# Performance work log

Hardware: AMD Instinct MI355X
Metric: run time of the kernel (lower is better)

The kernel has to match this reference:

```python
import jax, jax.numpy as jnp
import numpy as np

BS, CK, H, W, T = 4, 64, 32, 32, 16
HW = H * W
N = T * HW
CV = 256
TOP_K = 30


def setup_inputs() -> dict:
    key = jax.random.key(0)
    ks = jax.random.split(key, 16)
    inp = {
        'query_key': jax.random.normal(ks[0], (BS, CK, H, W), jnp.float32),
        'query_selection': jax.random.uniform(ks[1], (BS, CK, H, W), jnp.float32),
        'pix_feat': jax.random.normal(ks[2], (BS, CV, H, W), jnp.float32),
        'sensory': jax.random.normal(ks[3], (BS, CV, H, W), jnp.float32),
        'last_mask': jax.random.uniform(ks[4], (BS, 1, H, W), jnp.float32),
        'last_pix_feat': jax.random.normal(ks[5], (BS, CV, H, W), jnp.float32),
        'last_msk_value': jax.random.normal(ks[6], (BS, 1, CV, H, W), jnp.float32),
        'mem_key': jax.random.normal(ks[7], (BS, CK, N), jnp.float32),
        'mem_shrinkage': jax.random.uniform(ks[8], (BS, 1, N), jnp.float32),
        'mem_msk_value': jax.random.normal(ks[9], (BS, CV, N), jnp.float32),
        'mem_valid': jnp.ones((BS, N), jnp.float32),
        'obj_memory': jax.random.normal(ks[10], (BS, 1, 16, CV), jnp.float32),
        # uncertainty head proxy: 1x1 conv over concat(last_pix_feat, pix_feat, last_mask, diff)
        'W_uncert': jax.random.normal(ks[11], (1, CV + CV + 1 + CV), jnp.float32) * 0.02,
        'b_uncert': jnp.zeros((1,), jnp.float32),
    }
    return inp


def reference(query_key, query_selection, pix_feat, sensory, last_mask,
              last_pix_feat, last_msk_value, mem_key, mem_shrinkage,
              mem_msk_value, mem_valid, obj_memory, W_uncert, b_uncert):
    bs = query_key.shape[0]
    h, w = query_key.shape[-2:]
    hw = h * w
    qk = query_key.reshape(bs, CK, hw)            # [b,64,hw]
    qe = query_selection.reshape(bs, CK, hw)      # [b,64,hw]
    mk_t = jnp.swapaxes(mem_key, 1, 2)            # [b,N,64]
    # negative squared L2 distance, selection-weighted
    a_sq = jnp.einsum('bnc,bch->bnh', mk_t * mk_t, qe)
    two_ab = 2.0 * jnp.einsum('bnc,bch->bnh', mk_t, qk * qe)
    b_sq = jnp.sum(qe * qk * qk, axis=1, keepdims=True)     # [b,1,hw]
    sim = (-a_sq + two_ab - b_sq)                           # [b,N,hw]
    sim = sim * jnp.swapaxes(mem_shrinkage, 1, 2) / jnp.sqrt(jnp.float32(CK))
    sim = sim + (1.0 - mem_valid[..., None]) * -60000.0
    # top-k softmax over memory axis, scatter back to dense affinity
    sim_t = jnp.swapaxes(sim, 1, 2)                         # [b,hw,N]
    top_vals, top_idx = jax.lax.top_k(sim_t, TOP_K)         # [b,hw,k]
    probs = jax.nn.softmax(top_vals, axis=-1)
    b_ix = jnp.arange(bs)[:, None, None]
    q_ix = jnp.arange(hw)[None, :, None]
    aff = jnp.zeros_like(sim_t).at[b_ix, q_ix, top_idx].set(probs)  # [b,hw,N]
    visual = jnp.einsum('bcn,bhn->bch', mem_msk_value, aff).reshape(bs, 1, CV, h, w)
    # uncertainty-gated blend with last memory value (pred_uncertainty proxy: 1x1 conv)
    diff = visual[:, 0] - last_msk_value[:, 0]              # [b,256,h,w]
    feats = jnp.concatenate([last_pix_feat, pix_feat, last_mask, diff], axis=1)
    logits = jnp.einsum('bchw,oc->bohw', feats, W_uncert) + b_uncert[None, :, None, None]
    up = jax.nn.sigmoid(logits)[:, None]                    # [b,1,1,h,w]
    out = visual * up + last_msk_value * (1.0 - up)         # [b,1,256,h,w]
    return out
```

## Files before the change

kernel.cpp:

```cpp
#include <hip/hip_runtime.h>
#include <math.h>

#define BSZ 4
#define CKC 64
#define HWP 1024
#define NMEM 16384
#define CVC 256
#define PT 32
#define NT 128
#define NSPLIT 4
#define CHUNK (NMEM / NSPLIT)
#define NC (NSPLIT * 32)
#define PT2 16

#define WS_BQ_OFF    0
#define WS_BQ_SZ     (BSZ * 128 * HWP)
#define WS_BSQ_OFF   (WS_BQ_OFF + WS_BQ_SZ)
#define WS_BSQ_SZ    (BSZ * HWP)
#define WS_PRE_OFF   (WS_BSQ_OFF + WS_BSQ_SZ)
#define WS_PRE_SZ    (BSZ * HWP)
#define WS_PARTV_OFF (WS_PRE_OFF + WS_PRE_SZ)
#define WS_PARTV_SZ  (BSZ * HWP * NC)
#define WS_PARTI_OFF (WS_PARTV_OFF + WS_PARTV_SZ)
#define WS_PARTI_SZ  (BSZ * HWP * NC)
#define WS_VT_OFF    (WS_PARTI_OFF + WS_PARTI_SZ)
#define WS_VT_SZ     (BSZ * NMEM * CVC)
#define WS_TOTAL_FLOATS (WS_VT_OFF + WS_VT_SZ)

__global__ __launch_bounds__(256) void prep_kernel(
    const float* __restrict__ qk, const float* __restrict__ qe,
    const float* __restrict__ pf, const float* __restrict__ lm,
    const float* __restrict__ lpf, const float* __restrict__ lmv,
    const float* __restrict__ W, const float* __restrict__ bu,
    float* __restrict__ Bq, float* __restrict__ bsq, float* __restrict__ prelog)
{
    __shared__ float red[16][17];
    const int t  = threadIdx.x;
    const int b  = blockIdx.x >> 6;
    const int p0 = (blockIdx.x & 63) << 4;
    const int pp = t & 15;
    const int cg = t >> 4;
    const int p  = p0 + pp;

    const float* qkb = qk + (size_t)b * CKC * HWP;
    const float* qeb = qe + (size_t)b * CKC * HWP;
    float* Bqb = Bq + (size_t)b * 128 * HWP;

    float bs = 0.f;
    #pragma unroll
    for (int i = 0; i < 4; ++i) {
        const int cidx = (cg << 2) + i;
        const float k_ = qkb[cidx * HWP + p];
        const float e_ = qeb[cidx * HWP + p];
        Bqb[cidx * HWP + p]        = 2.f * k_ * e_;
        Bqb[(64 + cidx) * HWP + p] = -e_;
        bs += e_ * k_ * k_;
    }
    red[cg][pp] = bs;
    __syncthreads();
    if (t < 16) {
        float s = 0.f;
        #pragma unroll
        for (int g2 = 0; g2 < 16; ++g2) s += red[g2][t];
        bsq[b * HWP + p0 + t] = s;
    }
    const float* lpfb = lpf + (size_t)b * CVC * HWP;
    const float* pfb  = pf  + (size_t)b * CVC * HWP;
    const float* lmvb = lmv + (size_t)b * CVC * HWP;
    float lg = 0.f;
    #pragma unroll
    for (int i = 0; i < 16; ++i) {
        const int cidx = (cg << 4) + i;
        lg += W[cidx]       * lpfb[cidx * HWP + p];
        lg += W[256 + cidx] * pfb[cidx * HWP + p];
        lg -= W[513 + cidx] * lmvb[cidx * HWP + p];
    }
    __syncthreads();
    red[cg][pp] = lg;
    __syncthreads();
    if (t < 16) {
        float s = bu[0] + W[512] * lm[b * HWP + p0 + t];
        #pragma unroll
        for (int g2 = 0; g2 < 16; ++g2) s += red[g2][t];
        prelog[b * HWP + p0 + t] = s;
    }
}

__global__ __launch_bounds__(256) void transpose_v(const float* __restrict__ V,
                                                   float* __restrict__ VT)
{
    __shared__ float tile[32][33];
    const int b  = blockIdx.z;
    const int n0 = blockIdx.x << 5;
    const int c0 = blockIdx.y << 5;
    const int tx = threadIdx.x, ty = threadIdx.y;
    const float* Vb  = V  + (size_t)b * CVC * NMEM;
    float*       VTb = VT + (size_t)b * NMEM * CVC;
    #pragma unroll
    for (int i = 0; i < 32; i += 8)
        tile[ty + i][tx] = Vb[(size_t)(c0 + ty + i) * NMEM + n0 + tx];
    __syncthreads();
    #pragma unroll
    for (int i = 0; i < 32; i += 8)
        VTb[(size_t)(n0 + ty + i) * CVC + c0 + tx] = tile[tx][ty + i];
}

__global__ __launch_bounds__(256) void sim_topk_kernel(
    const float* __restrict__ mk, const float* __restrict__ shr,
    const float* __restrict__ valid, const float* __restrict__ Bq,
    const float* __restrict__ bsq,
    float* __restrict__ partV, float* __restrict__ partI)
{
    __shared__ float mkS[64][NT];
    __shared__ float fS[64][PT];
    __shared__ float gS[64][PT];
    __shared__ float heapV[PT][34];
    __shared__ int   heapI[PT][34];
    __shared__ float qV[PT][33];
    __shared__ int   qI[PT][33];
    __shared__ float shrS[NT];
    __shared__ float penS[NT];
    __shared__ float bsqS[PT];
    __shared__ int   qCnt[PT];
    __shared__ int   pendAny;

    const int t     = threadIdx.x;
    const int b     = blockIdx.x >> 7;
    const int pg    = (blockIdx.x >> 2) & 31;
    const int ns    = blockIdx.x & 3;
    const int p0    = pg << 5;
    const int nbase = ns * CHUNK;
    const int tn    = t & 31;
    const int tp    = t >> 5;

    const float* Bqb = Bq + (size_t)b * 128 * HWP;
    for (int idx = t; idx < 64 * PT; idx += 256) {
        const int c = idx >> 5, pp = idx & 31;
        fS[c][pp] = Bqb[c * HWP + p0 + pp];
        gS[c][pp] = Bqb[(64 + c) * HWP + p0 + pp];
    }
    if (t < PT) {
        bsqS[t] = bsq[b * HWP + p0 + t];
        qCnt[t] = 0;
    }
    if (t == 0) pendAny = 0;

    const float* mkb  = mk    + (size_t)b * CKC * NMEM;
    const float* shrb = shr   + (size_t)b * NMEM;
    const float* vlb  = valid + (size_t)b * NMEM;

    for (int ntile = 0; ntile < CHUNK / NT; ++ntile) {
        const int nstart = nbase + ntile * NT;
        if (t < NT) {
            shrS[t] = shrb[nstart + t] * 0.125f;
            penS[t] = (1.f - vlb[nstart + t]) * -60000.f;
        }
        #pragma unroll
        for (int k = 0; k < 8; ++k) {
            const int idx = t + (k << 8);
            const int row = idx >> 5;
            const int c4  = (idx & 31) << 2;
            *(float4*)&mkS[row][c4] =
                *(const float4*)&mkb[(size_t)row * NMEM + nstart + c4];
        }
        __syncthreads();

        float acc[4][4];
        #pragma unroll
        for (int i = 0; i < 4; ++i)
            #pragma unroll
            for (int j = 0; j < 4; ++j) acc[i][j] = 0.f;

        #pragma unroll 8
        for (int cc = 0; cc < 64; ++cc) {
            const float4 a4 = *(const float4*)&mkS[cc][tn << 2];
            const float4 f4 = *(const float4*)&fS[cc][tp << 2];
            const float4 g4 = *(const float4*)&gS[cc][tp << 2];
            const float m[4]  = {a4.x, a4.y, a4.z, a4.w};
            const float ff[4] = {f4.x, f4.y, f4.z, f4.w};
            const float gg[4] = {g4.x, g4.y, g4.z, g4.w};
            #pragma unroll
            for (int i = 0; i < 4; ++i) {
                const float mv = m[i];
                #pragma unroll
                for (int j = 0; j < 4; ++j) {
                    const float t1 = fmaf(mv, gg[j], ff[j]);
                    acc[i][j] = fmaf(mv, t1, acc[i][j]);
                }
            }
        }

        float simv[4][4];
        #pragma unroll
        for (int i = 0; i < 4; ++i) {
            const float sh = shrS[(tn << 2) + i];
            const float pe = penS[(tn << 2) + i];
            #pragma unroll
            for (int j = 0; j < 4; ++j)
                simv[i][j] = fmaf(acc[i][j] - bsqS[(tp << 2) + j], sh, pe);
        }

        unsigned pending = 0xFFFFu;
        if (ntile == 0) {
            if (tn < 8) {
                #pragma unroll
                for (int j = 0; j < 4; ++j) {
                    const int p = (tp << 2) + j;
                    #pragma unroll
                    for (int i = 0; i < 4; ++i) {
                        heapV[p][1 + (tn << 2) + i] = simv[i][j];
                        heapI[p][1 + (tn << 2) + i] = nbase + (tn << 2) + i;
                    }
                }
                pending = 0;
            }
            __syncthreads();
            if (t < PT) {
                for (int rt = 16; rt >= 1; --rt) {
                    const float v = heapV[t][rt];
                    const int  ix = heapI[t][rt];
                    int i = rt;
                    while (true) {
                        const int l = i << 1;
                        if (l > 32) break;
                        int m = l;
                        float vm = heapV[t][l];
                        if (l + 1 <= 32) {
                            const float vr = heapV[t][l + 1];
                            if (vr < vm) { m = l + 1; vm = vr; }
                        }
                        if (vm >= v) break;
                        heapV[t][i] = vm; heapI[t][i] = heapI[t][m];
                        i = m;
                    }
                    heapV[t][i] = v; heapI[t][i] = ix;
                }
            }
            __syncthreads();
        }

        while (true) {
            if (t == 0) pendAny = 0;
            if (t < PT) qCnt[t] = 0;
            __syncthreads();
            if (pending) {
                #pragma unroll
                for (int j = 0; j < 4; ++j) {
                    const int p = (tp << 2) + j;
                    const float mv = heapV[p][1];
                    #pragma unroll
                    for (int i = 0; i < 4; ++i) {
                        const unsigned bitm = 1u << ((j << 2) + i);
                        if (pending & bitm) {
                            const float v = simv[i][j];
                            if (v > mv) {
                                const int slot = atomicAdd(&qCnt[p], 1);
                                if (slot < 32) {
                                    qV[p][slot] = v;
                                    qI[p][slot] = nstart + (tn << 2) + i;
                                    pending &= ~bitm;
                                }
                            } else pending &= ~bitm;
                        }
                    }
                }
                if (pending) pendAny = 1;
            }
            __syncthreads();
            if (t < PT) {
                int cnt = qCnt[t]; if (cnt > 32) cnt = 32;
                for (int s = 0; s < cnt; ++s) {
                    const float v = qV[t][s];
                    if (v > heapV[t][1]) {
                        const int ix = qI[t][s];
                        int i = 1;
                        while (true) {
                            const int l = i << 1;
                            if (l > 32) break;
                            int m = l;
                            float vm = heapV[t][l];
                            if (l + 1 <= 32) {
                                const float vr = heapV[t][l + 1];
                                if (vr < vm) { m = l + 1; vm = vr; }
                            }
                            if (vm >= v) break;
                            heapV[t][i] = vm; heapI[t][i] = heapI[t][m];
                            i = m;
                        }
                        heapV[t][i] = v; heapI[t][i] = ix;
                    }
                }
            }
            __syncthreads();
            const int again = pendAny;
            __syncthreads();
            if (!again) break;
        }
    }

    for (int idx = t; idx < PT * 32; idx += 256) {
        const int p = idx >> 5, s = idx & 31;
        const size_t gp = (size_t)b * HWP + p0 + p;
        partV[gp * NC + ns * 32 + s] = heapV[p][1 + s];
        partI[gp * NC + ns * 32 + s] = (float)heapI[p][1 + s];
    }
}

__global__ __launch_bounds__(256) void merge_kernel(
    const float* __restrict__ partV, const float* __restrict__ partI,
    const float* __restrict__ Vv, const float* __restrict__ lmv,
    const float* __restrict__ prelog, const float* __restrict__ W,
    float* __restrict__ out, int use_vt)
{
    __shared__ float candV[PT2][NC + 1];
    __shared__ int   candI[PT2][NC + 1];
    __shared__ float hV[PT2][34];
    __shared__ int   hI[PT2][34];
    __shared__ float probS[PT2][33];
    __shared__ int   selS[PT2][33];
    __shared__ float prelS[PT2];
    __shared__ float partS[4][PT2];
    __shared__ float upS[PT2];
    __shared__ float visS[CVC][PT2 + 1];

    const int t  = threadIdx.x;
    const int b  = blockIdx.x >> 6;
    const int pg = blockIdx.x & 63;
    const int p0 = pg << 4;

    for (int idx = t; idx < PT2 * NC; idx += 256) {
        const int p = idx >> 7, s = idx & (NC - 1);
        const size_t gp = (size_t)b * HWP + p0 + p;
        candV[p][s] = partV[gp * NC + s];
        candI[p][s] = (int)partI[gp * NC + s];
    }
    if (t < PT2) prelS[t] = prelog[b * HWP + p0 + t];
    __syncthreads();

    if (t < PT2) {
        const int p = t;
        #pragma unroll
        for (int s = 0; s < 32; ++s) { hV[p][1 + s] = candV[p][s]; hI[p][1 + s] = candI[p][s]; }
        for (int rt = 16; rt >= 1; --rt) {
            const float v = hV[p][rt]; const int ix = hI[p][rt];
            int i = rt;
            while (true) {
                const int l = i << 1;
                if (l > 32) break;
                int m = l;
                float vm = hV[p][l];
                if (l + 1 <= 32) { const float vr = hV[p][l + 1]; if (vr < vm) { m = l + 1; vm = vr; } }
                if (vm >= v) break;
                hV[p][i] = vm; hI[p][i] = hI[p][m];
                i = m;
            }
            hV[p][i] = v; hI[p][i] = ix;
        }
        for (int s = 32; s < NC; ++s) {
            const float v = candV[p][s];
            if (v > hV[p][1]) {
                const int ix = candI[p][s];
                int i = 1;
                while (true) {
                    const int l = i << 1;
                    if (l > 32) break;
                    int m = l;
                    float vm = hV[p][l];
                    if (l + 1 <= 32) { const float vr = hV[p][l + 1]; if (vr < vm) { m = l + 1; vm = vr; } }
                    if (vm >= v) break;
                    hV[p][i] = vm; hI[p][i] = hI[p][m];
                    i = m;
                }
                hV[p][i] = v; hI[p][i] = ix;
            }
        }
        const int m1 = 1;
        const int m2 = (hV[p][3] < hV[p][2]) ? 3 : 2;
        float mx = hV[p][1];
        #pragma unroll
        for (int s = 2; s <= 32; ++s) mx = fmaxf(mx, hV[p][s]);
        float sum = 0.f;
        #pragma unroll
        for (int s = 1; s <= 32; ++s) {
            const float e = (s == m1 || s == m2) ? 0.f : expf(hV[p][s] - mx);
            probS[p][s - 1] = e; sum += e;
            selS[p][s - 1]  = hI[p][s];
        }
        const float inv = 1.f / sum;
        #pragma unroll
        for (int s = 0; s < 32; ++s) probS[p][s] *= inv;
    }
    __syncthreads();

    const int c  = t;
    const int ln = t & 63;
    const int wv = t >> 6;
    float vis[PT2];
    const float* Vb = Vv + (use_vt ? (size_t)b * NMEM * CVC : (size_t)b * CVC * NMEM);
    #pragma unroll
    for (int p = 0; p < PT2; ++p) {
        float a = 0.f;
        for (int s = 0; s < 32; ++s) {
            const float pr = probS[p][s];
            if (pr != 0.f) {
                const int idx = selS[p][s];
                const float v = use_vt ? Vb[(size_t)idx * CVC + c]
                                       : Vb[(size_t)c * NMEM + idx];
                a = fmaf(pr, v, a);
            }
        }
        vis[p] = a;
        visS[c][p] = a;
    }
    const float w3 = W[513 + c];
    #pragma unroll
    for (int p = 0; p < PT2; ++p) {
        float v = w3 * vis[p];
        #pragma unroll
        for (int off = 32; off > 0; off >>= 1) v += __shfl_xor(v, off, 64);
        if (ln == 0) partS[wv][p] = v;
    }
    __syncthreads();
    if (t < PT2) {
        const float lg = prelS[t] + partS[0][t] + partS[1][t] + partS[2][t] + partS[3][t];
        upS[t] = 1.f / (1.f + expf(-lg));
    }
    __syncthreads();

    const int pp = t & 15;
    const int cg = t >> 4;
    const float u = upS[pp];
    #pragma unroll
    for (int ci = 0; ci < 16; ++ci) {
        const int cc = (cg << 4) + ci;
        const float vv = visS[cc][pp];
        const size_t off = ((size_t)b * CVC + cc) * HWP + p0 + pp;
        out[off] = vv * u + lmv[off] * (1.f - u);
    }
}

extern "C" void kernel_launch(void* const* d_in, const int* in_sizes, int n_in,
                              void* d_out, int out_size, void* d_ws, size_t ws_size,
                              hipStream_t stream)
{
    const float* qk  = (const float*)d_in[0];
    const float* qe  = (const float*)d_in[1];
    const float* pf  = (const float*)d_in[2];
    const float* lm  = (const float*)d_in[4];
    const float* lpf = (const float*)d_in[5];
    const float* lmv = (const float*)d_in[6];
    const float* mk  = (const float*)d_in[7];
    const float* shr = (const float*)d_in[8];
    const float* Vv  = (const float*)d_in[9];
    const float* vld = (const float*)d_in[10];
    const float* W   = (const float*)d_in[12];
    const float* bu  = (const float*)d_in[13];
    float* out = (float*)d_out;
    float* ws  = (float*)d_ws;

    float* Bq     = ws + WS_BQ_OFF;
    float* bsq    = ws + WS_BSQ_OFF;
    float* prelog = ws + WS_PRE_OFF;
    float* partV  = ws + WS_PARTV_OFF;
    float* partI  = ws + WS_PARTI_OFF;
    float* VT     = ws + WS_VT_OFF;
    const int use_vt = (ws_size >= (size_t)WS_TOTAL_FLOATS * sizeof(float)) ? 1 : 0;

    prep_kernel<<<BSZ * 64, 256, 0, stream>>>(qk, qe, pf, lm, lpf, lmv, W, bu,
                                              Bq, bsq, prelog);
    if (use_vt)
        transpose_v<<<dim3(NMEM / 32, CVC / 32, BSZ), dim3(32, 8), 0, stream>>>(Vv, VT);
    sim_topk_kernel<<<BSZ * 32 * NSPLIT, 256, 0, stream>>>(mk, shr, vld, Bq, bsq,
                                                           partV, partI);
    merge_kernel<<<BSZ * 64, 256, 0, stream>>>(partV, partI, use_vt ? VT : Vv,
                                               lmv, prelog, W, out, use_vt);
}
```

Baseline: 800.3 us.

## Compute similarity with split-bf16 MFMA, pack operands, and split merge into select/gather kernels

Replaces the FP32 FMA similarity loop with bf16 MFMA 16x16x32 instructions. Memory keys and their squares are pre-packed into hi/lo bf16 pairs with a swizzled layout, and query operands are packed the same way. Key tiles are double-buffered into LDS with global_load_lds, and the split grows to 8 chunks with 64-pixel tiles. The value transpose now stores bf16, which halves gather traffic. The merge is split into a top-k select kernel and a gather/blend kernel. This trades extra pack passes and reduced precision (bf16 values, a three-term split product) for far higher matrix throughput, at some risk of different top-k selections near ties.

```diff
diff --git a/kernel.cpp b/kernel.cpp
--- a/kernel.cpp
+++ b/kernel.cpp
@@ -1,19 +1,27 @@
 #include <hip/hip_runtime.h>
 #include <math.h>
+
+typedef __attribute__((ext_vector_type(8))) short bf16x8;
+typedef __attribute__((ext_vector_type(4))) float f32x4;
 
 #define BSZ 4
 #define CKC 64
 #define HWP 1024
 #define NMEM 16384
 #define CVC 256
-#define PT 32
-#define NT 128
-#define NSPLIT 4
-#define CHUNK (NMEM / NSPLIT)
-#define NC (NSPLIT * 32)
-#define PT2 16
-
-#define WS_BQ_OFF    0
+
+#define NSPLIT 8
+#define CHUNK 2048
+#define NITER 16
+#define NC 256
+#define PT 64
+#define QC 18
+
+#define WS_APACK_OFF 0
+#define WS_APACK_SZ  8388608
+#define WS_BPACK_OFF (WS_APACK_OFF + WS_APACK_SZ)
+#define WS_BPACK_SZ  524288
+#define WS_BQ_OFF    (WS_BPACK_OFF + WS_BPACK_SZ)
 #define WS_BQ_SZ     (BSZ * 128 * HWP)
 #define WS_BSQ_OFF   (WS_BQ_OFF + WS_BQ_SZ)
 #define WS_BSQ_SZ    (BSZ * HWP)
@@ -23,9 +31,35 @@
 #define WS_PARTV_SZ  (BSZ * HWP * NC)
 #define WS_PARTI_OFF (WS_PARTV_OFF + WS_PARTV_SZ)
 #define WS_PARTI_SZ  (BSZ * HWP * NC)
-#define WS_VT_OFF    (WS_PARTI_OFF + WS_PARTI_SZ)
-#define WS_VT_SZ     (BSZ * NMEM * CVC)
+#define WS_SELP_OFF  (WS_PARTI_OFF + WS_PARTI_SZ)
+#define WS_SELP_SZ   (BSZ * HWP * 32)
+#define WS_SELI_OFF  (WS_SELP_OFF + WS_SELP_SZ)
+#define WS_SELI_SZ   (BSZ * HWP * 32)
+#define WS_VT_OFF    (WS_SELI_OFF + WS_SELI_SZ)
+#define WS_VT_SZ     8388608
 #define WS_TOTAL_FLOATS (WS_VT_OFF + WS_VT_SZ)
+
+__device__ __forceinline__ unsigned short f2bf(float x) {
+    unsigned u = __float_as_uint(x);
+    u = (u + 0x7FFFu + ((u >> 16) & 1u)) >> 16;
+    return (unsigned short)u;
+}
+__device__ __forceinline__ float bfhi(float x) {
+    unsigned u = __float_as_uint(x);
+    u = (u + 0x7FFFu + ((u >> 16) & 1u)) & 0xFFFF0000u;
+    return __uint_as_float(u);
+}
+
+__device__ __forceinline__ void gld16(const void* g, void* l) {
+    __builtin_amdgcn_global_load_lds(
+        (const __attribute__((address_space(1))) unsigned int*)g,
+        (__attribute__((address_space(3))) unsigned int*)l, 16, 0, 0);
+}
+
+#define BAR()  asm volatile("s_barrier" ::: "memory")
+#define LBAR() asm volatile("s_waitcnt lgkmcnt(0)\n\ts_barrier" ::: "memory")
+#define VM4()  asm volatile("s_waitcnt vmcnt(4)" ::: "memory")
+#define VM0()  asm volatile("s_waitcnt vmcnt(0)" ::: "memory")
 
 __global__ __launch_bounds__(256) void prep_kernel(
     const float* __restrict__ qk, const float* __restrict__ qe,
@@ -86,149 +120,246 @@
     }
 }
 
+__global__ __launch_bounds__(256) void pack_a(const float* __restrict__ mk,
+                                              unsigned int* __restrict__ Ap)
+{
+    __shared__ float ld[128][65];
+    const int t = threadIdx.x;
+    const int b = blockIdx.x >> 7;
+    const int nblk = blockIdx.x & 127;
+    const int n0 = nblk << 7;
+    const float* mkb = mk + (size_t)b * CKC * NMEM;
+    #pragma unroll
+    for (int k = 0; k < 8; ++k) {
+        const int i = t + (k << 8);
+        const int c = i >> 5;
+        const int f4 = i & 31;
+        const float4 v = *(const float4*)&mkb[(size_t)c * NMEM + n0 + (f4 << 2)];
+        ld[(f4 << 2) + 0][c] = v.x; ld[(f4 << 2) + 1][c] = v.y;
+        ld[(f4 << 2) + 2][c] = v.z; ld[(f4 << 2) + 3][c] = v.w;
+    }
+    __syncthreads();
+    const int r = t >> 1;
+    const int half = t & 1;
+    #pragma unroll
+    for (int kk = 0; kk < 2; ++kk) {
+        const int ks = half * 2 + kk;
+        const size_t tileByte = ((size_t)((b * 128 + nblk) * 4 + ks)) * 16384;
+        #pragma unroll
+        for (int g8 = 0; g8 < 4; ++g8) {
+            unsigned hi[8], lo[8];
+            #pragma unroll
+            for (int j = 0; j < 8; ++j) {
+                const int c = ks * 32 + g8 * 8 + j;
+                const float base = (c < 64) ? ld[r][c] : ld[r][c - 64];
+                const float x = (c < 64) ? base : base * base;
+                const float h = bfhi(x);
+                hi[j] = __float_as_uint(h) >> 16;
+                lo[j] = (unsigned)f2bf(x - h);
+            }
+            uint4 hv, lv;
+            hv.x = hi[0] | (hi[1] << 16); hv.y = hi[2] | (hi[3] << 16);
+            hv.z = hi[4] | (hi[5] << 16); hv.w = hi[6] | (hi[7] << 16);
+            lv.x = lo[0] | (lo[1] << 16); lv.y = lo[2] | (lo[3] << 16);
+            lv.z = lo[4] | (lo[5] << 16); lv.w = lo[6] | (lo[7] << 16);
+            const int sh = (g8 * 2 + 0) ^ (r & 7);
+            const int sl = (g8 * 2 + 1) ^ (r & 7);
+            *(uint4*)((char*)Ap + tileByte + r * 128 + sh * 16) = hv;
+            *(uint4*)((char*)Ap + tileByte + r * 128 + sl * 16) = lv;
+        }
+    }
+}
+
+__global__ __launch_bounds__(256) void pack_b(const float* __restrict__ Bq,
+                                              unsigned int* __restrict__ Bp)
+{
+    const int tid = blockIdx.x * 256 + threadIdx.x;
+    const int o = tid & 15;
+    const int p = (tid >> 4) & 1023;
+    const int b = tid >> 14;
+    const int ks = o >> 2, g = o & 3;
+    const float* Bqb = Bq + (size_t)b * 128 * HWP;
+    unsigned hi[8], lo[8];
+    #pragma unroll
+    for (int j = 0; j < 8; ++j) {
+        const int c = ks * 32 + g * 8 + j;
+        const float x = Bqb[(size_t)c * HWP + p];
+        const float h = bfhi(x);
+        hi[j] = __float_as_uint(h) >> 16;
+        lo[j] = (unsigned)f2bf(x - h);
+    }
+    uint4 hv, lv;
+    hv.x = hi[0] | (hi[1] << 16); hv.y = hi[2] | (hi[3] << 16);
+    hv.z = hi[4] | (hi[5] << 16); hv.w = hi[6] | (hi[7] << 16);
+    lv.x = lo[0] | (lo[1] << 16); lv.y = lo[2] | (lo[3] << 16);
+    lv.z = lo[4] | (lo[5] << 16); lv.w = lo[6] | (lo[7] << 16);
+    char* dst = (char*)Bp + ((size_t)(b * 1024 + p)) * 512 + ks * 128 + g * 32;
+    *(uint4*)(dst)      = hv;
+    *(uint4*)(dst + 16) = lv;
+}
+
 __global__ __launch_bounds__(256) void transpose_v(const float* __restrict__ V,
-                                                   float* __restrict__ VT)
+                                                   unsigned short* __restrict__ VT)
 {
     __shared__ float tile[32][33];
     const int b  = blockIdx.z;
     const int n0 = blockIdx.x << 5;
     const int c0 = blockIdx.y << 5;
     const int tx = threadIdx.x, ty = threadIdx.y;
-    const float* Vb  = V  + (size_t)b * CVC * NMEM;
-    float*       VTb = VT + (size_t)b * NMEM * CVC;
+    const float* Vb = V + (size_t)b * CVC * NMEM;
+    unsigned short* VTb = VT + (size_t)b * NMEM * CVC;
     #pragma unroll
     for (int i = 0; i < 32; i += 8)
         tile[ty + i][tx] = Vb[(size_t)(c0 + ty + i) * NMEM + n0 + tx];
     __syncthreads();
     #pragma unroll
     for (int i = 0; i < 32; i += 8)
-        VTb[(size_t)(n0 + ty + i) * CVC + c0 + tx] = tile[tx][ty + i];
-}
-
-__global__ __launch_bounds__(256) void sim_topk_kernel(
-    const float* __restrict__ mk, const float* __restrict__ shr,
-    const float* __restrict__ valid, const float* __restrict__ Bq,
+        VTb[(size_t)(n0 + ty + i) * CVC + c0 + tx] = f2bf(tile[tx][ty + i]);
+}
+
+__global__ __launch_bounds__(256) void sim_mfma(
+    const unsigned int* __restrict__ Ap, const unsigned int* __restrict__ Bp,
+    const float* __restrict__ shr, const float* __restrict__ valid,
     const float* __restrict__ bsq,
     float* __restrict__ partV, float* __restrict__ partI)
 {
-    __shared__ float mkS[64][NT];
-    __shared__ float fS[64][PT];
-    __shared__ float gS[64][PT];
-    __shared__ float heapV[PT][34];
-    __shared__ int   heapI[PT][34];
-    __shared__ float qV[PT][33];
-    __shared__ int   qI[PT][33];
-    __shared__ float shrS[NT];
-    __shared__ float penS[NT];
-    __shared__ float bsqS[PT];
-    __shared__ int   qCnt[PT];
-    __shared__ int   pendAny;
-
-    const int t     = threadIdx.x;
-    const int b     = blockIdx.x >> 7;
-    const int pg    = (blockIdx.x >> 2) & 31;
-    const int ns    = blockIdx.x & 3;
-    const int p0    = pg << 5;
-    const int nbase = ns * CHUNK;
-    const int tn    = t & 31;
-    const int tp    = t >> 5;
-
-    const float* Bqb = Bq + (size_t)b * 128 * HWP;
-    for (int idx = t; idx < 64 * PT; idx += 256) {
-        const int c = idx >> 5, pp = idx & 31;
-        fS[c][pp] = Bqb[c * HWP + p0 + pp];
-        gS[c][pp] = Bqb[(64 + c) * HWP + p0 + pp];
-    }
-    if (t < PT) {
-        bsqS[t] = bsq[b * HWP + p0 + t];
-        qCnt[t] = 0;
-    }
-    if (t == 0) pendAny = 0;
-
-    const float* mkb  = mk    + (size_t)b * CKC * NMEM;
-    const float* shrb = shr   + (size_t)b * NMEM;
-    const float* vlb  = valid + (size_t)b * NMEM;
-
-    for (int ntile = 0; ntile < CHUNK / NT; ++ntile) {
-        const int nstart = nbase + ntile * NT;
-        if (t < NT) {
-            shrS[t] = shrb[nstart + t] * 0.125f;
-            penS[t] = (1.f - vlb[nstart + t]) * -60000.f;
-        }
+    __shared__ bf16x8 Abuf[2][1024];
+    __shared__ float2 shrpenS[CHUNK];
+    __shared__ float  bsqS[64];
+    __shared__ float  heapV[64][33];
+    __shared__ int    heapI[64][33];
+    __shared__ float  qV[64][QC];
+    __shared__ int    qI[64][QC];
+    __shared__ int    qCnt[64];
+    __shared__ int    pendAny;
+
+    const int t = threadIdx.x;
+    const int bid = blockIdx.x;
+    const int wk = ((bid & 7) << 6) + (bid >> 3);
+    const int pg = wk & 15;
+    const int ns = (wk >> 4) & 7;
+    const int b  = wk >> 7;
+    const int p0 = pg << 6;
+    const int w  = t >> 6;
+    const int l  = t & 63;
+    const int wn = w >> 1;
+    const int wp = w & 1;
+    const int col = l & 15;
+    const int g   = l >> 4;
+
+    {
+        const float* shrb = shr   + (size_t)b * NMEM + ns * CHUNK;
+        const float* vlb  = valid + (size_t)b * NMEM + ns * CHUNK;
         #pragma unroll
         for (int k = 0; k < 8; ++k) {
-            const int idx = t + (k << 8);
-            const int row = idx >> 5;
-            const int c4  = (idx & 31) << 2;
-            *(float4*)&mkS[row][c4] =
-                *(const float4*)&mkb[(size_t)row * NMEM + nstart + c4];
-        }
-        __syncthreads();
-
-        float acc[4][4];
-        #pragma unroll
-        for (int i = 0; i < 4; ++i)
+            const int i = t + (k << 8);
+            shrpenS[i] = make_float2(shrb[i] * 0.125f, (1.f - vlb[i]) * -60000.f);
+        }
+        if (t < 64) { bsqS[t] = bsq[(size_t)b * HWP + p0 + t]; qCnt[t] = 0; }
+        if (t == 0) pendAny = 0;
+    }
+
+    bf16x8 Bf[2][4][2];
+    {
+        const char* BpB = (const char*)Bp;
+        #pragma unroll
+        for (int tj = 0; tj < 2; ++tj) {
+            const int p = p0 + wp * 32 + tj * 16 + col;
+            const char* base = BpB + ((size_t)(b * 1024 + p)) * 512 + g * 32;
             #pragma unroll
-            for (int j = 0; j < 4; ++j) acc[i][j] = 0.f;
-
-        #pragma unroll 8
-        for (int cc = 0; cc < 64; ++cc) {
-            const float4 a4 = *(const float4*)&mkS[cc][tn << 2];
-            const float4 f4 = *(const float4*)&fS[cc][tp << 2];
-            const float4 g4 = *(const float4*)&gS[cc][tp << 2];
-            const float m[4]  = {a4.x, a4.y, a4.z, a4.w};
-            const float ff[4] = {f4.x, f4.y, f4.z, f4.w};
-            const float gg[4] = {g4.x, g4.y, g4.z, g4.w};
+            for (int ks = 0; ks < 4; ++ks) {
+                Bf[tj][ks][0] = *(const bf16x8*)(base + ks * 128);
+                Bf[tj][ks][1] = *(const bf16x8*)(base + ks * 128 + 16);
+            }
+        }
+    }
+    __syncthreads();
+    const float bq[2] = { bsqS[wp * 32 + col], bsqS[wp * 32 + 16 + col] };
+
+    const char* ApB = (const char*)Ap + ((size_t)((b * 128 + ns * 16) * 4)) * 16384;
+    char* AbB = (char*)&Abuf[0][0];
+
+    #define STAGE(seqq) do {                                                   \
+        const char* gsrc_ = ApB + (size_t)(seqq) * 16384 + w * 4096 + l * 16;  \
+        char* ldst_ = AbB + (((seqq) & 1) << 14) + w * 4096;                   \
+        gld16(gsrc_,        ldst_);                                            \
+        gld16(gsrc_ + 1024, ldst_ + 1024);                                     \
+        gld16(gsrc_ + 2048, ldst_ + 2048);                                     \
+        gld16(gsrc_ + 3072, ldst_ + 3072);                                     \
+    } while (0)
+
+    STAGE(0);
+
+    for (int iter = 0; iter < NITER; ++iter) {
+        f32x4 acc[4][2];
+        #pragma unroll
+        for (int ti = 0; ti < 4; ++ti) {
+            acc[ti][0] = (f32x4){0.f, 0.f, 0.f, 0.f};
+            acc[ti][1] = (f32x4){0.f, 0.f, 0.f, 0.f};
+        }
+
+        #pragma unroll
+        for (int ks = 0; ks < 4; ++ks) {
+            const int seq = iter * 4 + ks;
+            BAR();
+            if (seq < 63) { STAGE(seq + 1); VM4(); }
+            else          { VM0(); }
+            BAR();
+            const bf16x8* Ab = &Abuf[0][0] + ((seq & 1) << 10);
             #pragma unroll
-            for (int i = 0; i < 4; ++i) {
-                const float mv = m[i];
+            for (int ti = 0; ti < 4; ++ti) {
+                const int r = wn * 64 + ti * 16 + col;
+                const bf16x8 aH = Ab[r * 8 + (((g << 1)    ) ^ (col & 7))];
+                const bf16x8 aL = Ab[r * 8 + (((g << 1) + 1) ^ (col & 7))];
                 #pragma unroll
-                for (int j = 0; j < 4; ++j) {
-                    const float t1 = fmaf(mv, gg[j], ff[j]);
-                    acc[i][j] = fmaf(mv, t1, acc[i][j]);
+                for (int tj = 0; tj < 2; ++tj) {
+                    acc[ti][tj] = __builtin_amdgcn_mfma_f32_16x16x32_bf16(aH, Bf[tj][ks][0], acc[ti][tj], 0, 0, 0);
+                    acc[ti][tj] = __builtin_amdgcn_mfma_f32_16x16x32_bf16(aH, Bf[tj][ks][1], acc[ti][tj], 0, 0, 0);
+                    acc[ti][tj] = __builtin_amdgcn_mfma_f32_16x16x32_bf16(aL, Bf[tj][ks][0], acc[ti][tj], 0, 0, 0);
                 }
             }
         }
 
-        float simv[4][4];
-        #pragma unroll
-        for (int i = 0; i < 4; ++i) {
-            const float sh = shrS[(tn << 2) + i];
-            const float pe = penS[(tn << 2) + i];
+        float simr[4][2][4];
+        #pragma unroll
+        for (int ti = 0; ti < 4; ++ti) {
             #pragma unroll
-            for (int j = 0; j < 4; ++j)
-                simv[i][j] = fmaf(acc[i][j] - bsqS[(tp << 2) + j], sh, pe);
-        }
-
-        unsigned pending = 0xFFFFu;
-        if (ntile == 0) {
-            if (tn < 8) {
+            for (int rr = 0; rr < 4; ++rr) {
+                const int nl = wn * 64 + ti * 16 + (g << 2) + rr;
+                const float2 sp = shrpenS[iter * 128 + nl];
                 #pragma unroll
-                for (int j = 0; j < 4; ++j) {
-                    const int p = (tp << 2) + j;
+                for (int tj = 0; tj < 2; ++tj)
+                    simr[ti][tj][rr] = fmaf(acc[ti][tj][rr] - bq[tj], sp.x, sp.y);
+            }
+        }
+
+        unsigned pend = 0xFFFFFFFFu;
+        if (iter == 0) {
+            if (wn == 0) {
+                #pragma unroll
+                for (int ti = 0; ti < 2; ++ti)
                     #pragma unroll
-                    for (int i = 0; i < 4; ++i) {
-                        heapV[p][1 + (tn << 2) + i] = simv[i][j];
-                        heapI[p][1 + (tn << 2) + i] = nbase + (tn << 2) + i;
+                    for (int tj = 0; tj < 2; ++tj) {
+                        const int pl = wp * 32 + tj * 16 + col;
+                        #pragma unroll
+                        for (int rr = 0; rr < 4; ++rr) {
+                            const int slot = ti * 16 + (g << 2) + rr + 1;
+                            heapV[pl][slot] = simr[ti][tj][rr];
+                            heapI[pl][slot] = ns * CHUNK + ti * 16 + (g << 2) + rr;
+                        }
                     }
-                }
-                pending = 0;
-            }
-            __syncthreads();
-            if (t < PT) {
+                pend = 0xFFFF0000u;
+            }
+            LBAR();
+            if (t < 64) {
                 for (int rt = 16; rt >= 1; --rt) {
-                    const float v = heapV[t][rt];
-                    const int  ix = heapI[t][rt];
+                    const float v = heapV[t][rt]; const int ix = heapI[t][rt];
                     int i = rt;
                     while (true) {
-                        const int l = i << 1;
-                        if (l > 32) break;
-                        int m = l;
-                        float vm = heapV[t][l];
-                        if (l + 1 <= 32) {
-                            const float vr = heapV[t][l + 1];
-                            if (vr < vm) { m = l + 1; vm = vr; }
-                        }
+                        const int lc = i << 1;
+                        if (lc > 32) break;
+                        int m = lc; float vm = heapV[t][lc];
+                        if (lc + 1 <= 32) { const float vr = heapV[t][lc + 1]; if (vr < vm) { m = lc + 1; vm = vr; } }
                         if (vm >= v) break;
                         heapV[t][i] = vm; heapI[t][i] = heapI[t][m];
                         i = m;
@@ -236,53 +367,52 @@
                     heapV[t][i] = v; heapI[t][i] = ix;
                 }
             }
-            __syncthreads();
+            LBAR();
         }
 
         while (true) {
             if (t == 0) pendAny = 0;
-            if (t < PT) qCnt[t] = 0;
-            __syncthreads();
-            if (pending) {
+            if (t < 64) qCnt[t] = 0;
+            LBAR();
+            if (pend) {
                 #pragma unroll
-                for (int j = 0; j < 4; ++j) {
-                    const int p = (tp << 2) + j;
-                    const float mv = heapV[p][1];
+                for (int tj = 0; tj < 2; ++tj) {
+                    const int pl = wp * 32 + tj * 16 + col;
+                    const float root = heapV[pl][1];
                     #pragma unroll
-                    for (int i = 0; i < 4; ++i) {
-                        const unsigned bitm = 1u << ((j << 2) + i);
-                        if (pending & bitm) {
-                            const float v = simv[i][j];
-                            if (v > mv) {
-                                const int slot = atomicAdd(&qCnt[p], 1);
-                                if (slot < 32) {
-                                    qV[p][slot] = v;
-                                    qI[p][slot] = nstart + (tn << 2) + i;
-                                    pending &= ~bitm;
-                                }
-                            } else pending &= ~bitm;
+                    for (int ti = 0; ti < 4; ++ti) {
+                        #pragma unroll
+                        for (int rr = 0; rr < 4; ++rr) {
+                            const unsigned bitm = 1u << (ti * 8 + tj * 4 + rr);
+                            if (pend & bitm) {
+                                const float v = simr[ti][tj][rr];
+                                if (v > root) {
+                                    const int s = atomicAdd(&qCnt[pl], 1);
+                                    if (s < QC) {
+                                        qV[pl][s] = v;
+                                        qI[pl][s] = ns * CHUNK + iter * 128 + wn * 64 + ti * 16 + (g << 2) + rr;
+                                        pend &= ~bitm;
+                                    }
+                                } else pend &= ~bitm;
+                            }
                         }
                     }
                 }
-                if (pending) pendAny = 1;
-            }
-            __syncthreads();
-            if (t < PT) {
-                int cnt = qCnt[t]; if (cnt > 32) cnt = 32;
+                if (pend) pendAny = 1;
+            }
+            LBAR();
+            if (t < 64) {
+                int cnt = qCnt[t]; if (cnt > QC) cnt = QC;
                 for (int s = 0; s < cnt; ++s) {
                     const float v = qV[t][s];
                     if (v > heapV[t][1]) {
                         const int ix = qI[t][s];
                         int i = 1;
                         while (true) {
-                            const int l = i << 1;
-                            if (l > 32) break;
-                            int m = l;
-                            float vm = heapV[t][l];
-                            if (l + 1 <= 32) {
-                                const float vr = heapV[t][l + 1];
-                                if (vr < vm) { m = l + 1; vm = vr; }
-                            }
+                            const int lc = i << 1;
+                            if (lc > 32) break;
+                            int m = lc; float vm = heapV[t][lc];
+                            if (lc + 1 <= 32) { const float vr = heapV[t][lc + 1]; if (vr < vm) { m = lc + 1; vm = vr; } }
                             if (vm >= v) break;
                             heapV[t][i] = vm; heapI[t][i] = heapI[t][m];
                             i = m;
@@ -291,53 +421,47 @@
                     }
                 }
             }
-            __syncthreads();
+            LBAR();
             const int again = pendAny;
-            __syncthreads();
+            LBAR();
             if (!again) break;
         }
     }
 
-    for (int idx = t; idx < PT * 32; idx += 256) {
+    for (int idx = t; idx < 64 * 32; idx += 256) {
         const int p = idx >> 5, s = idx & 31;
         const size_t gp = (size_t)b * HWP + p0 + p;
         partV[gp * NC + ns * 32 + s] = heapV[p][1 + s];
         partI[gp * NC + ns * 32 + s] = (float)heapI[p][1 + s];
     }
-}
-
-__global__ __launch_bounds__(256) void merge_kernel(
+    #undef STAGE
+}
+
+__global__ __launch_bounds__(256) void merge_select(
     const float* __restrict__ partV, const float* __restrict__ partI,
-    const float* __restrict__ Vv, const float* __restrict__ lmv,
-    const float* __restrict__ prelog, const float* __restrict__ W,
-    float* __restrict__ out, int use_vt)
-{
-    __shared__ float candV[PT2][NC + 1];
-    __shared__ int   candI[PT2][NC + 1];
-    __shared__ float hV[PT2][34];
-    __shared__ int   hI[PT2][34];
-    __shared__ float probS[PT2][33];
-    __shared__ int   selS[PT2][33];
-    __shared__ float prelS[PT2];
-    __shared__ float partS[4][PT2];
-    __shared__ float upS[PT2];
-    __shared__ float visS[CVC][PT2 + 1];
+    float* __restrict__ selP, int* __restrict__ selI)
+{
+    __shared__ float candV[16][NC + 1];
+    __shared__ int   candI[16][NC + 1];
+    __shared__ float hV[16][34];
+    __shared__ int   hI[16][34];
+    __shared__ float probS[16][33];
+    __shared__ int   selS[16][33];
 
     const int t  = threadIdx.x;
     const int b  = blockIdx.x >> 6;
     const int pg = blockIdx.x & 63;
     const int p0 = pg << 4;
 
-    for (int idx = t; idx < PT2 * NC; idx += 256) {
-        const int p = idx >> 7, s = idx & (NC - 1);
+    for (int idx = t; idx < 16 * NC; idx += 256) {
+        const int p = idx >> 8, s = idx & (NC - 1);
         const size_t gp = (size_t)b * HWP + p0 + p;
         candV[p][s] = partV[gp * NC + s];
         candI[p][s] = (int)partI[gp * NC + s];
     }
-    if (t < PT2) prelS[t] = prelog[b * HWP + p0 + t];
-    __syncthreads();
-
-    if (t < PT2) {
+    __syncthreads();
+
+    if (t < 16) {
         const int p = t;
         #pragma unroll
         for (int s = 0; s < 32; ++s) { hV[p][1 + s] = candV[p][s]; hI[p][1 + s] = candI[p][s]; }
@@ -345,11 +469,10 @@
             const float v = hV[p][rt]; const int ix = hI[p][rt];
             int i = rt;
             while (true) {
-                const int l = i << 1;
-                if (l > 32) break;
-                int m = l;
-                float vm = hV[p][l];
-                if (l + 1 <= 32) { const float vr = hV[p][l + 1]; if (vr < vm) { m = l + 1; vm = vr; } }
+                const int lc = i << 1;
+                if (lc > 32) break;
+                int m = lc; float vm = hV[p][lc];
+                if (lc + 1 <= 32) { const float vr = hV[p][lc + 1]; if (vr < vm) { m = lc + 1; vm = vr; } }
                 if (vm >= v) break;
                 hV[p][i] = vm; hI[p][i] = hI[p][m];
                 i = m;
@@ -362,11 +485,10 @@
                 const int ix = candI[p][s];
                 int i = 1;
                 while (true) {
-                    const int l = i << 1;
-                    if (l > 32) break;
-                    int m = l;
-                    float vm = hV[p][l];
-                    if (l + 1 <= 32) { const float vr = hV[p][l + 1]; if (vr < vm) { m = l + 1; vm = vr; } }
+                    const int lc = i << 1;
+                    if (lc > 32) break;
+                    int m = lc; float vm = hV[p][lc];
+                    if (lc + 1 <= 32) { const float vr = hV[p][lc + 1]; if (vr < vm) { m = lc + 1; vm = vr; } }
                     if (vm >= v) break;
                     hV[p][i] = vm; hI[p][i] = hI[p][m];
                     i = m;
@@ -392,20 +514,57 @@
     }
     __syncthreads();
 
+    for (int idx = t; idx < 512; idx += 256) {
+        const int p = idx >> 5, s = idx & 31;
+        const size_t gp = (size_t)b * HWP + p0 + p;
+        selP[gp * 32 + s] = probS[p][s];
+        selI[gp * 32 + s] = selS[p][s];
+    }
+}
+
+__global__ __launch_bounds__(256) void gather_blend(
+    const float* __restrict__ selP, const int* __restrict__ selI,
+    const unsigned short* __restrict__ VT, const float* __restrict__ Vv,
+    const float* __restrict__ lmv, const float* __restrict__ prelog,
+    const float* __restrict__ W, float* __restrict__ out, int use_vt)
+{
+    __shared__ float probS[16][33];
+    __shared__ int   selS[16][33];
+    __shared__ float prelS[16];
+    __shared__ float partS[4][16];
+    __shared__ float upS[16];
+    __shared__ float visS[CVC][17];
+
+    const int t  = threadIdx.x;
+    const int b  = blockIdx.x >> 6;
+    const int pg = blockIdx.x & 63;
+    const int p0 = pg << 4;
+
+    for (int idx = t; idx < 512; idx += 256) {
+        const int p = idx >> 5, s = idx & 31;
+        const size_t gp = (size_t)b * HWP + p0 + p;
+        probS[p][s] = selP[gp * 32 + s];
+        selS[p][s]  = selI[gp * 32 + s];
+    }
+    if (t < 16) prelS[t] = prelog[b * HWP + p0 + t];
+    __syncthreads();
+
     const int c  = t;
     const int ln = t & 63;
     const int wv = t >> 6;
-    float vis[PT2];
-    const float* Vb = Vv + (use_vt ? (size_t)b * NMEM * CVC : (size_t)b * CVC * NMEM);
-    #pragma unroll
-    for (int p = 0; p < PT2; ++p) {
+    float vis[16];
+    const unsigned short* VTb = VT + (size_t)b * NMEM * CVC;
+    const float* Vb = Vv + (size_t)b * CVC * NMEM;
+    #pragma unroll
+    for (int p = 0; p < 16; ++p) {
         float a = 0.f;
         for (int s = 0; s < 32; ++s) {
             const float pr = probS[p][s];
             if (pr != 0.f) {
                 const int idx = selS[p][s];
-                const float v = use_vt ? Vb[(size_t)idx * CVC + c]
-                                       : Vb[(size_t)c * NMEM + idx];
+                float v;
+                if (use_vt) v = __uint_as_float(((unsigned)VTb[(size_t)idx * CVC + c]) << 16);
+                else        v = Vb[(size_t)c * NMEM + idx];
                 a = fmaf(pr, v, a);
             }
         }
@@ -414,19 +573,18 @@
     }
     const float w3 = W[513 + c];
     #pragma unroll
-    for (int p = 0; p < PT2; ++p) {
+    for (int p = 0; p < 16; ++p) {
         float v = w3 * vis[p];
         #pragma unroll
         for (int off = 32; off > 0; off >>= 1) v += __shfl_xor(v, off, 64);
         if (ln == 0) partS[wv][p] = v;
     }
     __syncthreads();
-    if (t < PT2) {
+    if (t < 16) {
         const float lg = prelS[t] + partS[0][t] + partS[1][t] + partS[2][t] + partS[3][t];
         upS[t] = 1.f / (1.f + expf(-lg));
     }
     __syncthreads();
-
     const int pp = t & 15;
     const int cg = t >> 4;
     const float u = upS[pp];
@@ -458,20 +616,26 @@
     float* out = (float*)d_out;
     float* ws  = (float*)d_ws;
 
+    unsigned int* Apack = (unsigned int*)(ws + WS_APACK_OFF);
+    unsigned int* Bpack = (unsigned int*)(ws + WS_BPACK_OFF);
     float* Bq     = ws + WS_BQ_OFF;
     float* bsq    = ws + WS_BSQ_OFF;
     float* prelog = ws + WS_PRE_OFF;
     float* partV  = ws + WS_PARTV_OFF;
     float* partI  = ws + WS_PARTI_OFF;
-    float* VT     = ws + WS_VT_OFF;
+    float* selP   = ws + WS_SELP_OFF;
+    int*   selI   = (int*)(ws + WS_SELI_OFF);
+    unsigned short* VT = (unsigned short*)(ws + WS_VT_OFF);
     const int use_vt = (ws_size >= (size_t)WS_TOTAL_FLOATS * sizeof(float)) ? 1 : 0;
 
     prep_kernel<<<BSZ * 64, 256, 0, stream>>>(qk, qe, pf, lm, lpf, lmv, W, bu,
                                               Bq, bsq, prelog);
+    pack_a<<<BSZ * 128, 256, 0, stream>>>(mk, Apack);
+    pack_b<<<256, 256, 0, stream>>>(Bq, Bpack);
     if (use_vt)
         transpose_v<<<dim3(NMEM / 32, CVC / 32, BSZ), dim3(32, 8), 0, stream>>>(Vv, VT);
-    sim_topk_kernel<<<BSZ * 32 * NSPLIT, 256, 0, stream>>>(mk, shr, vld, Bq, bsq,
-                                                           partV, partI);
-    merge_kernel<<<BSZ * 64, 256, 0, stream>>>(partV, partI, use_vt ? VT : Vv,
-                                               lmv, prelog, W, out, use_vt);
-}
+    sim_mfma<<<512, 256, 0, stream>>>(Apack, Bpack, shr, vld, bsq, partV, partI);
+    merge_select<<<BSZ * 64, 256, 0, stream>>>(partV, partI, selP, selI);
+    gather_blend<<<BSZ * 64, 256, 0, stream>>>(selP, selI, VT, Vv, lmv, prelog,
+                                               W, out, use_vt);
+}
```

Result: faster. 671.5 us (-16.1%).
